# Optimization experiments

Hardware: AMD Instinct MI355X
Metric: run time of the kernel (lower is better)

## Reference

```python
import jax, jax.numpy as jnp
import numpy as np

EPS = 1e-5

def conv1x1(x, w, b):
    # x: [B,C,H,W], w: [O,C], b: [O]
    return jnp.einsum('bchw,oc->bohw', x, w) + b[None, :, None, None]

def bn_eval(x, w, b, m, v):
    inv = w / jnp.sqrt(v + EPS)
    return (x - m[None, :, None, None]) * inv[None, :, None, None] + b[None, :, None, None]

def setup_inputs() -> dict:
    key = jax.random.key(0)
    ks = jax.random.split(key, 32)
    B, Fg, Fl, Fi, H, W = 4, 128, 128, 64, 64, 64
    d = {}
    d['g'] = jax.random.normal(ks[0], (B, Fg, H, W), jnp.float32)
    d['x'] = jax.random.normal(ks[1], (B, Fl, H, W), jnp.float32)
    d['wg_w'] = jax.random.normal(ks[2], (Fi, Fg), jnp.float32) * 0.1
    d['wg_b'] = jax.random.normal(ks[3], (Fi,), jnp.float32) * 0.1
    d['bng_w'] = jax.random.uniform(ks[4], (Fi,), jnp.float32)
    d['bng_b'] = jax.random.normal(ks[5], (Fi,), jnp.float32) * 0.1
    d['bng_m'] = jax.random.normal(ks[6], (Fi,), jnp.float32) * 0.1
    d['bng_v'] = jax.random.uniform(ks[7], (Fi,), jnp.float32) + 0.5
    d['wx_w'] = jax.random.normal(ks[8], (Fi, Fl), jnp.float32) * 0.1
    d['wx_b'] = jax.random.normal(ks[9], (Fi,), jnp.float32) * 0.1
    d['bnx_w'] = jax.random.uniform(ks[10], (Fi,), jnp.float32)
    d['bnx_b'] = jax.random.normal(ks[11], (Fi,), jnp.float32) * 0.1
    d['bnx_m'] = jax.random.normal(ks[12], (Fi,), jnp.float32) * 0.1
    d['bnx_v'] = jax.random.uniform(ks[13], (Fi,), jnp.float32) + 0.5
    d['q_w'] = jax.random.normal(ks[14], (Fi // 8, Fi), jnp.float32) * 0.1
    d['q_b'] = jax.random.normal(ks[15], (Fi // 8,), jnp.float32) * 0.1
    d['k_w'] = jax.random.normal(ks[16], (Fi // 8, Fi), jnp.float32) * 0.1
    d['k_b'] = jax.random.normal(ks[17], (Fi // 8,), jnp.float32) * 0.1
    d['v_w'] = jax.random.normal(ks[18], (Fi, Fi), jnp.float32) * 0.1
    d['v_b'] = jax.random.normal(ks[19], (Fi,), jnp.float32) * 0.1
    d['sa_gamma'] = jax.random.normal(ks[20], (1,), jnp.float32)
    d['psi_w'] = jax.random.normal(ks[21], (1, Fi), jnp.float32) * 0.1
    d['psi_b'] = jax.random.normal(ks[22], (1,), jnp.float32) * 0.1
    d['bnp_w'] = jax.random.uniform(ks[23], (1,), jnp.float32)
    d['bnp_b'] = jax.random.normal(ks[24], (1,), jnp.float32) * 0.1
    d['bnp_m'] = jax.random.normal(ks[25], (1,), jnp.float32) * 0.1
    d['bnp_v'] = jax.random.uniform(ks[26], (1,), jnp.float32) + 0.5
    return d

def reference(g, x, wg_w, wg_b, bng_w, bng_b, bng_m, bng_v,
              wx_w, wx_b, bnx_w, bnx_b, bnx_m, bnx_v,
              q_w, q_b, k_w, k_b, v_w, v_b, sa_gamma,
              psi_w, psi_b, bnp_w, bnp_b, bnp_m, bnp_v):
    g1 = bn_eval(conv1x1(g, wg_w, wg_b), bng_w, bng_b, bng_m, bng_v)
    x1 = bn_eval(conv1x1(x, wx_w, wx_b), bnx_w, bnx_b, bnx_m, bnx_v)
    c = jax.nn.relu(g1 + x1)  # [B, Fi, H, W]
    B, C, H, W = c.shape
    N = H * W
    q = conv1x1(c, q_w, q_b).reshape(B, -1, N)  # [B, Fi/8, N]
    k = conv1x1(c, k_w, k_b).reshape(B, -1, N)
    v = conv1x1(c, v_w, v_b).reshape(B, C, N)
    energy = jnp.einsum('bcn,bcm->bnm', q, k)    # [B, N, N]
    attn = jax.nn.softmax(energy, axis=-1)
    sa_out = jnp.einsum('bcm,bnm->bcn', v, attn).reshape(B, C, H, W)
    attended = sa_gamma[0] * sa_out + c
    psi = jax.nn.sigmoid(bn_eval(conv1x1(attended, psi_w, psi_b), bnp_w, bnp_b, bnp_m, bnp_v))
    return x * psi
```

## Files before the change

kernel.cpp:

```cpp
#include <hip/hip_runtime.h>
#include <hip/hip_bf16.h>


typedef short bf16x8 __attribute__((ext_vector_type(8)));
typedef unsigned short u16x8 __attribute__((ext_vector_type(8)));
typedef unsigned short u16x4 __attribute__((ext_vector_type(4)));
typedef float f32x4 __attribute__((ext_vector_type(4)));

__device__ __forceinline__ unsigned short f2b16(float f) {
  return __builtin_bit_cast(unsigned short, __float2bfloat16(f));
}
__device__ __forceinline__ float b2f(unsigned short u) {
  return __bfloat162float(__builtin_bit_cast(__hip_bfloat16, u));
}

#define EPSV 1e-5f
#define LOG2E 1.44269504088896340736f

#define C_OFF      0u
#define Q_OFF      (C_OFF + 2097152u)
#define K_OFF      (Q_OFF + 262144u)
#define V_OFF      (K_OFF + 262144u)
#define OPART_OFF  (V_OFF + 2097152u)
#define ML_OFF     (OPART_OFF + 16777216u)

__global__ __launch_bounds__(256) void conv_fused_kernel(
    const float* __restrict__ g, const float* __restrict__ x,
    const float* __restrict__ wg_w, const float* __restrict__ wg_b,
    const float* __restrict__ bng_w, const float* __restrict__ bng_b,
    const float* __restrict__ bng_m, const float* __restrict__ bng_v,
    const float* __restrict__ wx_w, const float* __restrict__ wx_b,
    const float* __restrict__ bnx_w, const float* __restrict__ bnx_b,
    const float* __restrict__ bnx_m, const float* __restrict__ bnx_v,
    const float* __restrict__ q_w, const float* __restrict__ q_b,
    const float* __restrict__ k_w, const float* __restrict__ k_b,
    const float* __restrict__ v_w, const float* __restrict__ v_b,
    unsigned short* __restrict__ cb, unsigned short* __restrict__ Qb,
    unsigned short* __restrict__ Kb, unsigned short* __restrict__ Vb)
{
  __shared__ __attribute__((aligned(16))) unsigned short xt[16][264];
  __shared__ __attribute__((aligned(16))) unsigned short clds[16][72];
  __shared__ __attribute__((aligned(16))) unsigned short vstage[64][20];

  const int t = threadIdx.x;
  const int bid = blockIdx.x;
  const int b = bid >> 8;
  const int n0 = (bid & 255) << 4;

  {
    const int col4 = t & 3;
    const int rowg = t >> 2;
    float4 v[4];
    #pragma unroll
    for (int rr = 0; rr < 4; ++rr) {
      int row = rowg * 4 + rr;
      const float* src = (row < 128)
          ? (g + ((size_t)(b * 128 + row)) * 4096 + n0 + col4 * 4)
          : (x + ((size_t)(b * 128 + (row - 128))) * 4096 + n0 + col4 * 4);
      v[rr] = *(const float4*)src;
    }
    #pragma unroll
    for (int j = 0; j < 4; ++j) {
      u16x4 pk;
      #pragma unroll
      for (int rr = 0; rr < 4; ++rr)
        pk[rr] = f2b16(((const float*)&v[rr])[j]);
      *(u16x4*)(&xt[col4 * 4 + j][rowg * 4]) = pk;
    }
  }

  const int l = t & 63, w = t >> 6;
  const int l15 = l & 15, lg = l >> 4;
  f32x4 zf = {0.f, 0.f, 0.f, 0.f};

  const int orow = w * 16 + l15;
  const float invg = bng_w[orow] * rsqrtf(bng_v[orow] + EPSV);
  const float invx = bnx_w[orow] * rsqrtf(bnx_v[orow] + EPSV);
  bf16x8 afrag[8];
  #pragma unroll
  for (int ks = 0; ks < 8; ++ks) {
    int k = ks * 32 + lg * 8;
    const float* wp;
    float sc;
    if (k < 128) { wp = wg_w + orow * 128 + k;         sc = invg; }
    else         { wp = wx_w + orow * 128 + (k - 128); sc = invx; }
    float4 w0 = *(const float4*)wp;
    float4 w1 = *(const float4*)(wp + 4);
    u16x8 pk;
    pk[0] = f2b16(w0.x * sc); pk[1] = f2b16(w0.y * sc);
    pk[2] = f2b16(w0.z * sc); pk[3] = f2b16(w0.w * sc);
    pk[4] = f2b16(w1.x * sc); pk[5] = f2b16(w1.y * sc);
    pk[6] = f2b16(w1.z * sc); pk[7] = f2b16(w1.w * sc);
    afrag[ks] = __builtin_bit_cast(bf16x8, pk);
  }
  __syncthreads();

  f32x4 acc = zf;
  #pragma unroll
  for (int ks = 0; ks < 8; ++ks) {
    bf16x8 bfv = *(const bf16x8*)(&xt[l15][ks * 32 + lg * 8]);
    acc = __builtin_amdgcn_mfma_f32_16x16x32_bf16(afrag[ks], bfv, acc, 0, 0, 0);
  }
  #pragma unroll
  for (int r = 0; r < 4; ++r) {
    int o = w * 16 + lg * 4 + r;
    float ig = bng_w[o] * rsqrtf(bng_v[o] + EPSV);
    float ix = bnx_w[o] * rsqrtf(bnx_v[o] + EPSV);
    float bc = (wg_b[o] - bng_m[o]) * ig + bng_b[o]
             + (wx_b[o] - bnx_m[o]) * ix + bnx_b[o];
    float cv = fmaxf(acc[r] + bc, 0.f);
    unsigned short cv16 = f2b16(cv);
    cb[((size_t)(b * 64 + o)) * 4096 + n0 + l15] = cv16;
    clds[l15][o] = cv16;
  }
  __syncthreads();

  const int ngl = n0 + l15;
  #pragma unroll
  for (int i = 0; i < 2; ++i) {
    int t5 = w + 4 * i;
    if (t5 >= 5) break;
    int wrow = t5 * 16 + l15;
    f32x4 a2 = zf;
    #pragma unroll
    for (int kk = 0; kk < 2; ++kk) {
      int k = kk * 32 + lg * 8;
      const float* wp = (wrow < 8)  ? (q_w + wrow * 64 + k)
                      : (wrow < 16) ? (k_w + (wrow - 8) * 64 + k)
                                    : (v_w + (wrow - 16) * 64 + k);
      float4 w0 = *(const float4*)wp;
      float4 w1 = *(const float4*)(wp + 4);
      u16x8 pk;
      pk[0] = f2b16(w0.x); pk[1] = f2b16(w0.y);
      pk[2] = f2b16(w0.z); pk[3] = f2b16(w0.w);
      pk[4] = f2b16(w1.x); pk[5] = f2b16(w1.y);
      pk[6] = f2b16(w1.z); pk[7] = f2b16(w1.w);
      bf16x8 bfv = *(const bf16x8*)(&clds[l15][k]);
      a2 = __builtin_amdgcn_mfma_f32_16x16x32_bf16(
          __builtin_bit_cast(bf16x8, pk), bfv, a2, 0, 0, 0);
    }
    if (t5 == 0) {
      u16x4 pk;
      #pragma unroll
      for (int r = 0; r < 4; ++r) {
        int row = lg * 4 + r;
        float val;
        if (row < 8) val = (a2[r] + q_b[row]) * LOG2E;
        else         val = a2[r] + k_b[row - 8];
        pk[r] = f2b16(val);
      }
      if (lg < 2)
        *(u16x4*)(Qb + (((size_t)b << 12) + ngl) * 8 + lg * 4) = pk;
      else
        *(u16x4*)(Kb + (((size_t)b << 12) + ngl) * 8 + (lg - 2) * 4) = pk;
    } else {
      #pragma unroll
      for (int r = 0; r < 4; ++r) {
        int vch = (t5 - 1) * 16 + lg * 4 + r;
        vstage[vch][l15] = f2b16(a2[r] + v_b[vch]);
      }
    }
  }
  __syncthreads();

  {
    int row = t >> 2, seg = t & 3;
    u16x4 pv = *(const u16x4*)(&vstage[row][seg * 4]);
    *(u16x4*)(Vb + ((size_t)(b * 64 + row)) * 4096 + n0 + seg * 4) = pv;
  }
}

__global__ __launch_bounds__(256) void attn_partial_kernel(
    const unsigned short* __restrict__ Qb, const unsigned short* __restrict__ Kb,
    const unsigned short* __restrict__ Vb,
    unsigned short* __restrict__ Opart, float* __restrict__ ml)
{
  __shared__ __attribute__((aligned(16))) unsigned short klds[64][8];
  __shared__ __attribute__((aligned(16))) unsigned short vlds[64][72];
  __shared__ __attribute__((aligned(16))) unsigned short plds[4][2][16][40];

  const int t = threadIdx.x;
  const int bid = blockIdx.x;
  const int qt = bid & 63;
  const int b = (bid >> 6) & 3;
  const int ci = bid >> 8;
  const int n0 = qt << 6;
  const int l = t & 63, w = t >> 6;
  const int l15 = l & 15, lg = l >> 4;

  bf16x8 qf = {0, 0, 0, 0, 0, 0, 0, 0};
  if (lg == 0)
    qf = *(const bf16x8*)(Qb + (((size_t)b << 12) + n0 + w * 16 + l15) * 8);

  f32x4 zf = {0.f, 0.f, 0.f, 0.f};
  f32x4 O[4];
  O[0] = O[1] = O[2] = O[3] = zf;
  float m_run = -INFINITY;
  float l_run = 0.f;

  const int m_lo = ci << 9, m_hi = (ci + 1) << 9;
  for (int m0 = m_lo; m0 < m_hi; m0 += 64) {
    if (t < 64)
      *(int4*)(&klds[t][0]) = *(const int4*)(Kb + (((size_t)b << 12) + m0 + t) * 8);
    #pragma unroll
    for (int i = 0; i < 2; ++i) {
      int ci2 = t + 256 * i;
      int row = ci2 >> 3, off = ci2 & 7;
      *(int4*)(&vlds[row][off * 8]) =
          *(const int4*)(Vb + ((size_t)(b * 64 + row)) * 4096 + m0 + off * 8);
    }
    __syncthreads();

    f32x4 e[4];
    #pragma unroll
    for (int mt = 0; mt < 4; ++mt) {
      bf16x8 kf = *(const bf16x8*)(&klds[mt * 16 + l15][0]);
      e[mt] = __builtin_amdgcn_mfma_f32_16x16x32_bf16(kf, qf, zf, 0, 0, 0);
    }

    float vm = fmaxf(fmaxf(fmaxf(e[0][0], e[0][1]), fmaxf(e[0][2], e[0][3])),
                     fmaxf(fmaxf(e[1][0], e[1][1]), fmaxf(e[1][2], e[1][3])));
    float vm2 = fmaxf(fmaxf(fmaxf(e[2][0], e[2][1]), fmaxf(e[2][2], e[2][3])),
                      fmaxf(fmaxf(e[3][0], e[3][1]), fmaxf(e[3][2], e[3][3])));
    vm = fmaxf(vm, vm2);
    vm = fmaxf(vm, __shfl_xor(vm, 16));
    vm = fmaxf(vm, __shfl_xor(vm, 32));

    bool nosk = __any(vm > m_run + 8.f);
    float nm = nosk ? fmaxf(m_run, vm) : m_run;
    float s = 0.f;
    #pragma unroll
    for (int mt = 0; mt < 4; ++mt) {
      #pragma unroll
      for (int r = 0; r < 4; ++r) {
        float p = __builtin_amdgcn_exp2f(e[mt][r] - nm);
        e[mt][r] = p;
        s += p;
      }
    }
    s += __shfl_xor(s, 16);
    s += __shfl_xor(s, 32);
    if (nosk) {
      float sc = __builtin_amdgcn_exp2f(m_run - nm);
      l_run = l_run * sc + s;
      m_run = nm;
      #pragma unroll
      for (int ct = 0; ct < 4; ++ct)
        #pragma unroll
        for (int r = 0; r < 4; ++r) O[ct][r] *= sc;
    } else {
      l_run += s;
    }

    #pragma unroll
    for (int mt = 0; mt < 4; ++mt) {
      u16x4 pk;
      #pragma unroll
      for (int r = 0; r < 4; ++r) pk[r] = f2b16(e[mt][r]);
      int kk = mt >> 1;
      int lgr = 2 * (mt & 1) + (lg >> 1);
      int j0 = 4 * (lg & 1);
      *(u16x4*)(&plds[w][kk][l15][lgr * 8 + j0]) = pk;
    }

    #pragma unroll
    for (int ct = 0; ct < 4; ++ct) {
      #pragma unroll
      for (int kk = 0; kk < 2; ++kk) {
        bf16x8 pfr = *(const bf16x8*)(&plds[w][kk][l15][lg * 8]);
        bf16x8 vf = *(const bf16x8*)(&vlds[ct * 16 + l15][kk * 32 + lg * 8]);
        O[ct] = __builtin_amdgcn_mfma_f32_16x16x32_bf16(vf, pfr, O[ct], 0, 0, 0);
      }
    }
    __syncthreads();
  }

  const size_t pb = ((size_t)(ci * 4 + b)) << 12;
  const int qg = n0 + w * 16 + l15;
  #pragma unroll
  for (int ct = 0; ct < 4; ++ct) {
    u16x4 pk;
    #pragma unroll
    for (int r = 0; r < 4; ++r) pk[r] = f2b16(O[ct][r]);
    *(u16x4*)(Opart + (pb + qg) * 64 + ct * 16 + lg * 4) = pk;
  }
  if (lg == 0) {
    float2 mv;
    mv.x = m_run; mv.y = l_run;
    *(float2*)(ml + (pb + qg) * 2) = mv;
  }
}

__global__ __launch_bounds__(256) void combine_kernel(
    const unsigned short* __restrict__ Opart, const float* __restrict__ ml,
    const unsigned short* __restrict__ cb, const float* __restrict__ xin,
    const float* __restrict__ psi_w, const float* __restrict__ psi_b,
    const float* __restrict__ bnp_w, const float* __restrict__ bnp_b,
    const float* __restrict__ bnp_m, const float* __restrict__ bnp_v,
    const float* __restrict__ sa_gamma,
    float* __restrict__ out)
{
  __shared__ __attribute__((aligned(16))) unsigned short c_lds[64][20];
  __shared__ __attribute__((aligned(8))) float2 ml_lds[16][8];
  __shared__ float psi_lds[16];

  const int t = threadIdx.x;
  const int bid = blockIdx.x;
  const int b = bid >> 8;
  const int n0 = (bid & 255) << 4;

  {
    int row = t >> 2, seg = t & 3;
    *(u16x4*)(&c_lds[row][seg * 4]) =
        *(const u16x4*)(cb + ((size_t)(b * 64 + row)) * 4096 + n0 + seg * 4);
  }
  if (t < 128) {
    int q = t >> 3, ci = t & 7;
    ml_lds[q][ci] = *(const float2*)(ml + ((((size_t)(ci * 4 + b)) << 12) + n0 + q) * 2);
  }
  __syncthreads();

  const float invp = bnp_w[0] * rsqrtf(bnp_v[0] + EPSV);
  const float psi_c = (psi_b[0] - bnp_m[0]) * invp + bnp_b[0];
  const float gamma = sa_gamma[0];

  const int q = t >> 4, cg = t & 15;
  const int qg = n0 + q;

  float M = -INFINITY;
  #pragma unroll
  for (int ci = 0; ci < 8; ++ci) M = fmaxf(M, ml_lds[q][ci].x);
  float L = 0.f, wgt[8];
  #pragma unroll
  for (int ci = 0; ci < 8; ++ci) {
    wgt[ci] = __builtin_amdgcn_exp2f(ml_lds[q][ci].x - M);
    L += wgt[ci] * ml_lds[q][ci].y;
  }
  float o4[4] = {0.f, 0.f, 0.f, 0.f};
  #pragma unroll
  for (int ci = 0; ci < 8; ++ci) {
    u16x4 p = *(const u16x4*)(Opart + ((((size_t)(ci * 4 + b)) << 12) + qg) * 64 + cg * 4);
    float wv = wgt[ci];
    #pragma unroll
    for (int k = 0; k < 4; ++k) o4[k] += wv * b2f(p[k]);
  }
  const float invL = 1.f / L;
  float ps = 0.f;
  #pragma unroll
  for (int k = 0; k < 4; ++k) {
    int ch = cg * 4 + k;
    ps += (psi_w[ch] * invp) * (gamma * (o4[k] * invL) + b2f(c_lds[ch][q]));
  }
  ps += __shfl_xor(ps, 1);
  ps += __shfl_xor(ps, 2);
  ps += __shfl_xor(ps, 4);
  ps += __shfl_xor(ps, 8);
  if (cg == 0)
    psi_lds[q] = 1.f / (1.f + __expf(-(ps + psi_c)));
  __syncthreads();

  #pragma unroll
  for (int i = 0; i < 2; ++i) {
    int idx = t + 256 * i;
    int f = idx >> 2, c4 = idx & 3;
    size_t off = ((size_t)(b * 128 + f)) * 4096 + n0 + c4 * 4;
    float4 xv = *(const float4*)(xin + off);
    float4 ov;
    ov.x = xv.x * psi_lds[c4 * 4 + 0];
    ov.y = xv.y * psi_lds[c4 * 4 + 1];
    ov.z = xv.z * psi_lds[c4 * 4 + 2];
    ov.w = xv.w * psi_lds[c4 * 4 + 3];
    *(float4*)(out + off) = ov;
  }
}

extern "C" void kernel_launch(void* const* d_in, const int* in_sizes, int n_in,
                              void* d_out, int out_size, void* d_ws, size_t ws_size,
                              hipStream_t stream) {
  (void)in_sizes; (void)n_in; (void)out_size; (void)ws_size;
  const float* g     = (const float*)d_in[0];
  const float* x     = (const float*)d_in[1];
  const float* wg_w  = (const float*)d_in[2];
  const float* wg_b  = (const float*)d_in[3];
  const float* bng_w = (const float*)d_in[4];
  const float* bng_b = (const float*)d_in[5];
  const float* bng_m = (const float*)d_in[6];
  const float* bng_v = (const float*)d_in[7];
  const float* wx_w  = (const float*)d_in[8];
  const float* wx_b  = (const float*)d_in[9];
  const float* bnx_w = (const float*)d_in[10];
  const float* bnx_b = (const float*)d_in[11];
  const float* bnx_m = (const float*)d_in[12];
  const float* bnx_v = (const float*)d_in[13];
  const float* q_w   = (const float*)d_in[14];
  const float* q_b   = (const float*)d_in[15];
  const float* k_w   = (const float*)d_in[16];
  const float* k_b   = (const float*)d_in[17];
  const float* v_w   = (const float*)d_in[18];
  const float* v_b   = (const float*)d_in[19];
  const float* sa_g  = (const float*)d_in[20];
  const float* psi_w = (const float*)d_in[21];
  const float* psi_b = (const float*)d_in[22];
  const float* bnp_w = (const float*)d_in[23];
  const float* bnp_b = (const float*)d_in[24];
  const float* bnp_m = (const float*)d_in[25];
  const float* bnp_v = (const float*)d_in[26];
  float* out = (float*)d_out;

  char* ws = (char*)d_ws;
  unsigned short* cb = (unsigned short*)(ws + C_OFF);
  unsigned short* Qb = (unsigned short*)(ws + Q_OFF);
  unsigned short* Kb = (unsigned short*)(ws + K_OFF);
  unsigned short* Vb = (unsigned short*)(ws + V_OFF);
  unsigned short* Opart = (unsigned short*)(ws + OPART_OFF);
  float* mlb = (float*)(ws + ML_OFF);

  hipLaunchKernelGGL(conv_fused_kernel, dim3(1024), dim3(256), 0, stream,
                     g, x, wg_w, wg_b, bng_w, bng_b, bng_m, bng_v,
                     wx_w, wx_b, bnx_w, bnx_b, bnx_m, bnx_v,
                     q_w, q_b, k_w, k_b, v_w, v_b,
                     cb, Qb, Kb, Vb);

  hipLaunchKernelGGL(attn_partial_kernel, dim3(2048), dim3(256), 0, stream,
                     Qb, Kb, Vb, Opart, mlb);

  hipLaunchKernelGGL(combine_kernel, dim3(1024), dim3(256), 0, stream,
                     Opart, mlb, cb, x,
                     psi_w, psi_b, bnp_w, bnp_b, bnp_m, bnp_v, sa_g,
                     out);
}
```

Before: 172.9 us.

## Read K/V fragments directly from global in attention; widen conv tile to 32 columns

The attention partial kernel stops staging K and V tiles through LDS with block-wide barriers and instead has each lane load its MFMA fragments straight from global memory, relying on L1/L2 caching. This removes two __syncthreads per iteration and the LDS round trip, at the cost of more redundant global loads across waves. Separately, the conv kernel now handles 32 spatial columns per block instead of 16, halving the grid. This reuses the converted weight fragments across two MFMA tiles.

```diff
diff --git a/kernel.cpp b/kernel.cpp
--- a/kernel.cpp
+++ b/kernel.cpp
@@ -38,22 +38,22 @@
     unsigned short* __restrict__ cb, unsigned short* __restrict__ Qb,
     unsigned short* __restrict__ Kb, unsigned short* __restrict__ Vb)
 {
-  __shared__ __attribute__((aligned(16))) unsigned short xt[16][264];
-  __shared__ __attribute__((aligned(16))) unsigned short clds[16][72];
-  __shared__ __attribute__((aligned(16))) unsigned short vstage[64][20];
+  __shared__ __attribute__((aligned(16))) unsigned short xt[32][264];
+  __shared__ __attribute__((aligned(16))) unsigned short clds[32][72];
+  __shared__ __attribute__((aligned(16))) unsigned short vstage[64][36];
 
   const int t = threadIdx.x;
   const int bid = blockIdx.x;
-  const int b = bid >> 8;
-  const int n0 = (bid & 255) << 4;
+  const int b = bid >> 7;
+  const int n0 = (bid & 127) << 5;
 
   {
-    const int col4 = t & 3;
-    const int rowg = t >> 2;
-    float4 v[4];
-    #pragma unroll
-    for (int rr = 0; rr < 4; ++rr) {
-      int row = rowg * 4 + rr;
+    const int col4 = t & 7;
+    const int rowg = t >> 3;
+    float4 v[8];
+    #pragma unroll
+    for (int rr = 0; rr < 8; ++rr) {
+      int row = rowg * 8 + rr;
       const float* src = (row < 128)
           ? (g + ((size_t)(b * 128 + row)) * 4096 + n0 + col4 * 4)
           : (x + ((size_t)(b * 128 + (row - 128))) * 4096 + n0 + col4 * 4);
@@ -61,11 +61,11 @@
     }
     #pragma unroll
     for (int j = 0; j < 4; ++j) {
-      u16x4 pk;
-      #pragma unroll
-      for (int rr = 0; rr < 4; ++rr)
+      u16x8 pk;
+      #pragma unroll
+      for (int rr = 0; rr < 8; ++rr)
         pk[rr] = f2b16(((const float*)&v[rr])[j]);
-      *(u16x4*)(&xt[col4 * 4 + j][rowg * 4]) = pk;
+      *(u16x8*)(&xt[col4 * 4 + j][rowg * 8]) = pk;
     }
   }
 
@@ -95,11 +95,15 @@
   }
   __syncthreads();
 
-  f32x4 acc = zf;
+  f32x4 acc[2];
+  acc[0] = acc[1] = zf;
   #pragma unroll
   for (int ks = 0; ks < 8; ++ks) {
-    bf16x8 bfv = *(const bf16x8*)(&xt[l15][ks * 32 + lg * 8]);
-    acc = __builtin_amdgcn_mfma_f32_16x16x32_bf16(afrag[ks], bfv, acc, 0, 0, 0);
+    #pragma unroll
+    for (int ns = 0; ns < 2; ++ns) {
+      bf16x8 bfv = *(const bf16x8*)(&xt[ns * 16 + l15][ks * 32 + lg * 8]);
+      acc[ns] = __builtin_amdgcn_mfma_f32_16x16x32_bf16(afrag[ks], bfv, acc[ns], 0, 0, 0);
+    }
   }
   #pragma unroll
   for (int r = 0; r < 4; ++r) {
@@ -108,18 +112,21 @@
     float ix = bnx_w[o] * rsqrtf(bnx_v[o] + EPSV);
     float bc = (wg_b[o] - bng_m[o]) * ig + bng_b[o]
              + (wx_b[o] - bnx_m[o]) * ix + bnx_b[o];
-    float cv = fmaxf(acc[r] + bc, 0.f);
-    unsigned short cv16 = f2b16(cv);
-    cb[((size_t)(b * 64 + o)) * 4096 + n0 + l15] = cv16;
-    clds[l15][o] = cv16;
+    #pragma unroll
+    for (int ns = 0; ns < 2; ++ns) {
+      float cv = fmaxf(acc[ns][r] + bc, 0.f);
+      unsigned short cv16 = f2b16(cv);
+      cb[((size_t)(b * 64 + o)) * 4096 + n0 + ns * 16 + l15] = cv16;
+      clds[ns * 16 + l15][o] = cv16;
+    }
   }
   __syncthreads();
 
-  const int ngl = n0 + l15;
-  #pragma unroll
-  for (int i = 0; i < 2; ++i) {
-    int t5 = w + 4 * i;
-    if (t5 >= 5) break;
+  #pragma unroll
+  for (int i = 0; i < 3; ++i) {
+    int tau = w + 4 * i;
+    if (tau >= 10) break;
+    int t5 = tau % 5, ns = tau / 5;
     int wrow = t5 * 16 + l15;
     f32x4 a2 = zf;
     #pragma unroll
@@ -135,10 +142,11 @@
       pk[2] = f2b16(w0.z); pk[3] = f2b16(w0.w);
       pk[4] = f2b16(w1.x); pk[5] = f2b16(w1.y);
       pk[6] = f2b16(w1.z); pk[7] = f2b16(w1.w);
-      bf16x8 bfv = *(const bf16x8*)(&clds[l15][k]);
+      bf16x8 bfv = *(const bf16x8*)(&clds[ns * 16 + l15][k]);
       a2 = __builtin_amdgcn_mfma_f32_16x16x32_bf16(
           __builtin_bit_cast(bf16x8, pk), bfv, a2, 0, 0, 0);
     }
+    int ngl = n0 + ns * 16 + l15;
     if (t5 == 0) {
       u16x4 pk;
       #pragma unroll
@@ -157,14 +165,16 @@
       #pragma unroll
       for (int r = 0; r < 4; ++r) {
         int vch = (t5 - 1) * 16 + lg * 4 + r;
-        vstage[vch][l15] = f2b16(a2[r] + v_b[vch]);
+        vstage[vch][ns * 16 + l15] = f2b16(a2[r] + v_b[vch]);
       }
     }
   }
   __syncthreads();
 
-  {
-    int row = t >> 2, seg = t & 3;
+  #pragma unroll
+  for (int i = 0; i < 2; ++i) {
+    int idx = t + 256 * i;
+    int row = idx >> 3, seg = idx & 7;
     u16x4 pv = *(const u16x4*)(&vstage[row][seg * 4]);
     *(u16x4*)(Vb + ((size_t)(b * 64 + row)) * 4096 + n0 + seg * 4) = pv;
   }
@@ -175,8 +185,6 @@
     const unsigned short* __restrict__ Vb,
     unsigned short* __restrict__ Opart, float* __restrict__ ml)
 {
-  __shared__ __attribute__((aligned(16))) unsigned short klds[64][8];
-  __shared__ __attribute__((aligned(16))) unsigned short vlds[64][72];
   __shared__ __attribute__((aligned(16))) unsigned short plds[4][2][16][40];
 
   const int t = threadIdx.x;
@@ -198,23 +206,15 @@
   float m_run = -INFINITY;
   float l_run = 0.f;
 
+  const unsigned short* Kb_b = Kb + (((size_t)b << 12) + l15) * 8;
+  const unsigned short* Vb_b = Vb + ((size_t)(b * 64 + l15)) * 4096 + lg * 8;
+
   const int m_lo = ci << 9, m_hi = (ci + 1) << 9;
   for (int m0 = m_lo; m0 < m_hi; m0 += 64) {
-    if (t < 64)
-      *(int4*)(&klds[t][0]) = *(const int4*)(Kb + (((size_t)b << 12) + m0 + t) * 8);
-    #pragma unroll
-    for (int i = 0; i < 2; ++i) {
-      int ci2 = t + 256 * i;
-      int row = ci2 >> 3, off = ci2 & 7;
-      *(int4*)(&vlds[row][off * 8]) =
-          *(const int4*)(Vb + ((size_t)(b * 64 + row)) * 4096 + m0 + off * 8);
-    }
-    __syncthreads();
-
     f32x4 e[4];
     #pragma unroll
     for (int mt = 0; mt < 4; ++mt) {
-      bf16x8 kf = *(const bf16x8*)(&klds[mt * 16 + l15][0]);
+      bf16x8 kf = *(const bf16x8*)(Kb_b + (size_t)(m0 + mt * 16) * 8);
       e[mt] = __builtin_amdgcn_mfma_f32_16x16x32_bf16(kf, qf, zf, 0, 0, 0);
     }
 
@@ -267,12 +267,11 @@
     for (int ct = 0; ct < 4; ++ct) {
       #pragma unroll
       for (int kk = 0; kk < 2; ++kk) {
+        bf16x8 vf = *(const bf16x8*)(Vb_b + (size_t)ct * 16 * 4096 + m0 + kk * 32);
         bf16x8 pfr = *(const bf16x8*)(&plds[w][kk][l15][lg * 8]);
-        bf16x8 vf = *(const bf16x8*)(&vlds[ct * 16 + l15][kk * 32 + lg * 8]);
         O[ct] = __builtin_amdgcn_mfma_f32_16x16x32_bf16(vf, pfr, O[ct], 0, 0, 0);
       }
     }
-    __syncthreads();
   }
 
   const size_t pb = ((size_t)(ci * 4 + b)) << 12;
@@ -415,7 +414,7 @@
   unsigned short* Opart = (unsigned short*)(ws + OPART_OFF);
   float* mlb = (float*)(ws + ML_OFF);
 
-  hipLaunchKernelGGL(conv_fused_kernel, dim3(1024), dim3(256), 0, stream,
+  hipLaunchKernelGGL(conv_fused_kernel, dim3(512), dim3(256), 0, stream,
                      g, x, wg_w, wg_b, bng_w, bng_b, bng_m, bng_v,
                      wx_w, wx_b, bnx_w, bnx_b, bnx_m, bnx_v,
                      q_w, q_b, k_w, k_b, v_w, v_b,
```

Result: slower. 206.0 us (+19.1%).
